# Performance work log

Hardware: AMD Instinct MI355X
Metric: run time of the kernel (lower is better)

## Reference

```python
import jax, jax.numpy as jnp
import numpy as np
import math

E = 1024   # embed_dim
H = 16     # num_heads
D = E // H # head_dim


def _rotary(x):
    # x: [B, H, S, D]. Faithful to the original quirky implementation:
    # pos_enc[:, 0::2] = sin(position * div_term), then cos/sin are taken OF that value.
    S = x.shape[2]
    position = jnp.arange(S, dtype=jnp.float32)[:, None]                     # [S,1]
    div_term = jnp.exp(jnp.arange(0, D, 2, dtype=jnp.float32) * (-math.log(10000.0) / D))  # [D/2]
    angle = jnp.sin(position * div_term)                                     # [S, D/2] == pos_enc[:,0::2]
    cos_t = jnp.cos(angle)                                                   # [S, D/2]
    sin_t = jnp.sin(angle)                                                   # [S, D/2]
    xe = x[..., 0::2]
    xo = x[..., 1::2]
    re = xe * cos_t - xo * sin_t
    ro = xo * cos_t + xe * sin_t
    # interleave even/odd back: [..., D/2, 2] -> [..., D]
    return jnp.stack([re, ro], axis=-1).reshape(x.shape)


def setup_inputs() -> dict:
    key = jax.random.key(0)
    ks = jax.random.split(key, 12)
    B, S = 4, 1024
    scale = 1.0 / math.sqrt(E)
    inp = {
        "query": jax.random.normal(ks[0], (B, S, E), dtype=jnp.float32),
        "key":   jax.random.normal(ks[1], (B, S, E), dtype=jnp.float32),
        "value": jax.random.normal(ks[2], (B, S, E), dtype=jnp.float32),
        # Linear params stored as [in, out]; y = x @ W + b
        "Wq": jax.random.normal(ks[3], (E, E), dtype=jnp.float32) * scale,
        "bq": jnp.zeros((E,), dtype=jnp.float32),
        "Wk": jax.random.normal(ks[4], (E, E), dtype=jnp.float32) * scale,
        "bk": jnp.zeros((E,), dtype=jnp.float32),
        "Wv": jax.random.normal(ks[5], (E, E), dtype=jnp.float32) * scale,
        "bv": jnp.zeros((E,), dtype=jnp.float32),
        "Wo": jax.random.normal(ks[6], (E, E), dtype=jnp.float32) * scale,
        "bo": jnp.zeros((E,), dtype=jnp.float32),
    }
    return inp


def reference(query, key, value, Wq, bq, Wk, bk, Wv, bv, Wo, bo):
    B, S, _ = query.shape
    # projections -> [B, H, S, D]
    q = (query @ Wq + bq).reshape(B, S, H, D).transpose(0, 2, 1, 3)
    k = (key   @ Wk + bk).reshape(B, S, H, D).transpose(0, 2, 1, 3)
    v = (value @ Wv + bv).reshape(B, S, H, D).transpose(0, 2, 1, 3)
    q = _rotary(q)
    k = _rotary(k)
    scores = jnp.einsum('bhsd,bhtd->bhst', q, k) / (D ** 0.5)  # [B,H,S,S]
    probs = jax.nn.softmax(scores, axis=-1)
    # dropout p=0 (eval) -> identity
    ctx = jnp.einsum('bhst,bhtd->bhsd', probs, v)              # [B,H,S,D]
    ctx = ctx.transpose(0, 2, 1, 3).reshape(B, S, E)
    out = ctx @ Wo + bo
    return out, probs
```

## Files before the change

kernel.cpp:

```cpp
#include <hip/hip_runtime.h>
#include <hip/hip_bf16.h>

typedef __attribute__((ext_vector_type(8))) short bf16x8;
typedef __attribute__((ext_vector_type(4))) float f32x4;
typedef unsigned short u16;

__device__ __forceinline__ u16 f2bf(float f) {
  unsigned u = __float_as_uint(f);
  u += 0x7fffu + ((u >> 16) & 1u);
  return (u16)(u >> 16);
}

__device__ __forceinline__ void gload16(const void* g, void* l) {
  __builtin_amdgcn_global_load_lds(
      (const __attribute__((address_space(1))) unsigned int*)g,
      (__attribute__((address_space(3))) unsigned int*)l, 16, 0, 0);
}

__device__ __forceinline__ void blockbar() {
  asm volatile("" ::: "memory");
  __builtin_amdgcn_s_barrier();
  asm volatile("" ::: "memory");
}

__global__ __launch_bounds__(256) void prep_kernel(
    const float* __restrict__ query, const float* __restrict__ key_,
    const float* __restrict__ value, u16* __restrict__ qin,
    u16* __restrict__ kin, u16* __restrict__ vin,
    const float* __restrict__ Wq, const float* __restrict__ Wk,
    const float* __restrict__ Wv, const float* __restrict__ Wo,
    u16* __restrict__ WqT, u16* __restrict__ WkT, u16* __restrict__ WvT,
    u16* __restrict__ WoT, float* __restrict__ cosT, float* __restrict__ sinT) {
  __shared__ float tile[32][33];
  const int z = blockIdx.z;
  const int bx = blockIdx.x;
  const int tid = threadIdx.x;
  if (z < 3) {
    const float* in = z == 0 ? query : z == 1 ? key_ : value;
    u16* out = z == 0 ? qin : z == 1 ? kin : vin;
    size_t i = ((size_t)bx * 256 + tid) * 4;
    float4 v = *(const float4*)(in + i);
    ushort4 o = make_ushort4(f2bf(v.x), f2bf(v.y), f2bf(v.z), f2bf(v.w));
    *(ushort4*)(out + i) = o;
  } else if (z == 3) {
    const int w = bx >> 10;
    const float* W = w == 0 ? Wq : w == 1 ? Wk : w == 2 ? Wv : Wo;
    u16* Wt = w == 0 ? WqT : w == 1 ? WkT : w == 2 ? WvT : WoT;
    int tx = tid & 31, ty = tid >> 5;
    int k0 = ((bx >> 5) & 31) * 32, n0 = (bx & 31) * 32;
#pragma unroll
    for (int i = 0; i < 4; ++i)
      tile[ty + i * 8][tx] = W[(size_t)(k0 + ty + i * 8) * 1024 + n0 + tx];
    __syncthreads();
#pragma unroll
    for (int i = 0; i < 4; ++i)
      Wt[(size_t)(n0 + ty + i * 8) * 1024 + k0 + tx] = f2bf(tile[tx][ty + i * 8]);
  } else {
    int i = bx * 256 + tid;
    if (i >= 1024 * 32) return;
    int s = i >> 5, p = i & 31;
    double freq = exp(-9.210340371976184 * (double)(2 * p) / 64.0);
    double ang = sin((double)s * freq);
    cosT[i] = (float)cos(ang);
    sinT[i] = (float)sin(ang);
  }
}

__global__ __launch_bounds__(256) void proj_gemm_kernel(
    const u16* __restrict__ qin, const u16* __restrict__ kin,
    const u16* __restrict__ vin, const u16* __restrict__ WqT,
    const u16* __restrict__ WkT, const u16* __restrict__ WvT,
    const float* __restrict__ bq, const float* __restrict__ bk,
    const float* __restrict__ bv, u16* __restrict__ qr, u16* __restrict__ kr,
    u16* __restrict__ vt, const float* __restrict__ cosT,
    const float* __restrict__ sinT) {
  __shared__ u16 lA[2][128 * 32];
  __shared__ u16 lB[2][128 * 32];
  const int z = blockIdx.z;
  const u16* A = z == 0 ? qin : z == 1 ? kin : vin;
  const u16* Bt = z == 0 ? WqT : z == 1 ? WkT : WvT;
  const float* bias = z == 0 ? bq : z == 1 ? bk : bv;

  const int tid = threadIdx.x;
  const int lane = tid & 63, wid = tid >> 6;
  const int wm = wid >> 1, wn = wid & 1;
  const int lr = lane & 15, kg = lane >> 4;
  const int m0 = blockIdx.y * 128, n0 = blockIdx.x * 128;

  auto stage = [&](int bu, int k0) {
#pragma unroll
    for (int it = 0; it < 2; ++it) {
      int o = tid * 16 + it * 4096;
      int row = o >> 6;
      int cbs = (((o >> 4) & 3) ^ (row & 3)) << 4;
      gload16((const char*)A + ((size_t)(m0 + row) * 1024 + k0) * 2 + cbs,
              (char*)lA[bu] + o);
      gload16((const char*)Bt + ((size_t)(n0 + row) * 1024 + k0) * 2 + cbs,
              (char*)lB[bu] + o);
    }
  };

  stage(0, 0);
  f32x4 acc[4][4] = {};
  for (int t = 0; t < 32; ++t) {
    if (t < 31) {
      stage((t + 1) & 1, (t + 1) * 32);
      asm volatile("s_waitcnt vmcnt(4)" ::: "memory");
    } else {
      asm volatile("s_waitcnt vmcnt(0)" ::: "memory");
    }
    blockbar();
    const int cb = t & 1;
    bf16x8 av[4], bv_[4];
#pragma unroll
    for (int i = 0; i < 4; ++i) {
      int ra = wm * 64 + i * 16 + lr;
      av[i] = *(const bf16x8*)((const char*)lA[cb] + ra * 64 + ((kg ^ (ra & 3)) << 4));
      int rb = wn * 64 + i * 16 + lr;
      bv_[i] = *(const bf16x8*)((const char*)lB[cb] + rb * 64 + ((kg ^ (rb & 3)) << 4));
    }
#pragma unroll
    for (int i = 0; i < 4; ++i)
#pragma unroll
      for (int j = 0; j < 4; ++j)
        acc[i][j] = __builtin_amdgcn_mfma_f32_16x16x32_bf16(av[i], bv_[j], acc[i][j], 0, 0, 0);
    blockbar();
  }

  if (z == 2) {
    const int bb = m0 >> 10;
#pragma unroll
    for (int i = 0; i < 4; ++i) {
      int srow = (m0 & 1023) + wm * 64 + i * 16 + kg * 4;
#pragma unroll
      for (int j = 0; j < 4; ++j) {
        int col = n0 + wn * 64 + j * 16 + lr;
        float bcol = bias[col];
        int h = col >> 6, d = col & 63;
        ushort4 o;
        o.x = f2bf(acc[i][j][0] + bcol);
        o.y = f2bf(acc[i][j][1] + bcol);
        o.z = f2bf(acc[i][j][2] + bcol);
        o.w = f2bf(acc[i][j][3] + bcol);
        *(ushort4*)(vt + ((size_t)((bb * 16 + h) * 64 + d)) * 1024 + srow) = o;
      }
    }
  } else {
    u16* Cout = z == 0 ? qr : kr;
#pragma unroll
    for (int i = 0; i < 4; ++i) {
#pragma unroll
      for (int j = 0; j < 4; ++j) {
        int col = n0 + wn * 64 + j * 16 + lr;
        float bcol = bias[col];
#pragma unroll
        for (int r = 0; r < 4; ++r) {
          int row = m0 + wm * 64 + i * 16 + kg * 4 + r;
          float v = acc[i][j][r] + bcol;
          float pv = __shfl_xor(v, 1);
          int p = (col & 63) >> 1;
          int s = row & 1023;
          float ct = cosT[s * 32 + p], st = sinT[s * 32 + p];
          float ov = (col & 1) ? (v * ct + pv * st) : (v * ct - pv * st);
          Cout[(size_t)row * 1024 + col] = f2bf(ov);
        }
      }
    }
  }
}

__global__ __launch_bounds__(256) void out_gemm_kernel(
    const u16* __restrict__ A, const u16* __restrict__ Bt,
    const float* __restrict__ bias, float* __restrict__ Cout) {
  __shared__ u16 lA[2][128 * 32];
  __shared__ u16 lB[2][128 * 32];
  const int tid = threadIdx.x;
  const int lane = tid & 63, wid = tid >> 6;
  const int wm = wid >> 1, wn = wid & 1;
  const int lr = lane & 15, kg = lane >> 4;
  const int m0 = blockIdx.y * 128, n0 = blockIdx.x * 128;

  auto stage = [&](int bu, int k0) {
#pragma unroll
    for (int it = 0; it < 2; ++it) {
      int o = tid * 16 + it * 4096;
      int row = o >> 6;
      int cbs = (((o >> 4) & 3) ^ (row & 3)) << 4;
      gload16((const char*)A + ((size_t)(m0 + row) * 1024 + k0) * 2 + cbs,
              (char*)lA[bu] + o);
      gload16((const char*)Bt + ((size_t)(n0 + row) * 1024 + k0) * 2 + cbs,
              (char*)lB[bu] + o);
    }
  };

  stage(0, 0);
  f32x4 acc[4][4] = {};
  for (int t = 0; t < 32; ++t) {
    if (t < 31) {
      stage((t + 1) & 1, (t + 1) * 32);
      asm volatile("s_waitcnt vmcnt(4)" ::: "memory");
    } else {
      asm volatile("s_waitcnt vmcnt(0)" ::: "memory");
    }
    blockbar();
    const int cb = t & 1;
    bf16x8 av[4], bv_[4];
#pragma unroll
    for (int i = 0; i < 4; ++i) {
      int ra = wm * 64 + i * 16 + lr;
      av[i] = *(const bf16x8*)((const char*)lA[cb] + ra * 64 + ((kg ^ (ra & 3)) << 4));
      int rb = wn * 64 + i * 16 + lr;
      bv_[i] = *(const bf16x8*)((const char*)lB[cb] + rb * 64 + ((kg ^ (rb & 3)) << 4));
    }
#pragma unroll
    for (int i = 0; i < 4; ++i)
#pragma unroll
      for (int j = 0; j < 4; ++j)
        acc[i][j] = __builtin_amdgcn_mfma_f32_16x16x32_bf16(av[i], bv_[j], acc[i][j], 0, 0, 0);
    blockbar();
  }
#pragma unroll
  for (int i = 0; i < 4; ++i)
#pragma unroll
    for (int j = 0; j < 4; ++j) {
      int col = n0 + wn * 64 + j * 16 + lr;
      float bcol = bias[col];
#pragma unroll
      for (int r = 0; r < 4; ++r) {
        int row = m0 + wm * 64 + i * 16 + kg * 4 + r;
        Cout[(size_t)row * 1024 + col] = acc[i][j][r] + bcol;
      }
    }
}

__global__ __launch_bounds__(512, 4) void fused_attn_kernel(
    const u16* __restrict__ qr, const u16* __restrict__ kr,
    const u16* __restrict__ vt, float* __restrict__ probs,
    u16* __restrict__ ctx) {
  __shared__ u16 lQ[32 * 64];
  __shared__ u16 lK[2][128 * 64];
  __shared__ u16 lV[2][64 * 128];
  __shared__ u16 lP[32 * 128];
  __shared__ float redM[8][32];
  __shared__ float redS[8][32];

  const int tid = threadIdx.x;
  const int lane = tid & 63, wid = tid >> 6;
  const int lr = lane & 15, kg = lane >> 4;
  const int z = blockIdx.x, b = z >> 4, h = z & 15;
  const int m0 = blockIdx.y * 32;

  const char* Qb = (const char*)qr + ((size_t)(b * 1024 + m0) * 1024 + h * 64) * 2;
  const char* Kb = (const char*)kr + ((size_t)(b * 1024) * 1024 + h * 64) * 2;
  const char* Vb = (const char*)vt + (size_t)z * 64 * 1024 * 2;

  auto stageK = [&](int bu, int c) {
#pragma unroll
    for (int it = 0; it < 2; ++it) {
      int o = tid * 16 + it * 8192;
      int row = o >> 7, ch = (o >> 4) & 7;
      gload16(Kb + (size_t)(c * 128 + row) * 2048 + ((ch ^ (row & 7)) << 4),
              (char*)lK[bu] + o);
    }
  };
  auto stageV = [&](int bu, int c) {
#pragma unroll
    for (int it = 0; it < 2; ++it) {
      int o = tid * 16 + it * 8192;
      int row = o >> 8, ch = (o >> 4) & 15;
      gload16(Vb + (size_t)row * 2048 + c * 256 + ((ch ^ (row & 15)) << 4),
              (char*)lV[bu] + o);
    }
  };

  if (tid < 256) {
    int o = tid * 16;
    int row = o >> 7, ch = (o >> 4) & 7;
    gload16(Qb + (size_t)row * 2048 + ((ch ^ (row & 7)) << 4), (char*)lQ + o);
  }
  stageK(0, 0);

  bf16x8 qf[2][2];
  f32x4 accS[8][2] = {};
#pragma unroll
  for (int c = 0; c < 8; ++c) {
    if (c < 7) {
      stageK((c + 1) & 1, c + 1);
      asm volatile("s_waitcnt vmcnt(2)" ::: "memory");
    } else {
      asm volatile("s_waitcnt vmcnt(0)" ::: "memory");
    }
    blockbar();
    if (c == 0) {
#pragma unroll
      for (int ii = 0; ii < 2; ++ii)
#pragma unroll
        for (int ks = 0; ks < 2; ++ks) {
          int ra = ii * 16 + lr;
          int cc = ks * 4 + kg;
          qf[ii][ks] = *(const bf16x8*)((const char*)lQ + ra * 128 + ((cc ^ (ra & 7)) << 4));
        }
    }
    __builtin_amdgcn_s_setprio(1);
#pragma unroll
    for (int ks = 0; ks < 2; ++ks) {
      int rb = wid * 16 + lr;
      bf16x8 kf =
          *(const bf16x8*)((const char*)lK[c & 1] + rb * 128 + (((ks * 4 + kg) ^ (rb & 7)) << 4));
#pragma unroll
      for (int ii = 0; ii < 2; ++ii)
        accS[c][ii] =
            __builtin_amdgcn_mfma_f32_16x16x32_bf16(qf[ii][ks], kf, accS[c][ii], 0, 0, 0);
    }
    __builtin_amdgcn_s_setprio(0);
    blockbar();
  }

  stageV(0, 0);

  float rmax[2][4];
#pragma unroll
  for (int ii = 0; ii < 2; ++ii)
#pragma unroll
    for (int r = 0; r < 4; ++r) rmax[ii][r] = -1e30f;
#pragma unroll
  for (int c = 0; c < 8; ++c)
#pragma unroll
    for (int ii = 0; ii < 2; ++ii)
#pragma unroll
      for (int r = 0; r < 4; ++r) {
        float v = accS[c][ii][r] * 0.125f;
        accS[c][ii][r] = v;
        rmax[ii][r] = fmaxf(rmax[ii][r], v);
      }
#pragma unroll
  for (int ii = 0; ii < 2; ++ii)
#pragma unroll
    for (int r = 0; r < 4; ++r) {
      float v = rmax[ii][r];
      v = fmaxf(v, __shfl_xor(v, 1));
      v = fmaxf(v, __shfl_xor(v, 2));
      v = fmaxf(v, __shfl_xor(v, 4));
      v = fmaxf(v, __shfl_xor(v, 8));
      rmax[ii][r] = v;
    }
  if (lr == 0) {
#pragma unroll
    for (int ii = 0; ii < 2; ++ii)
#pragma unroll
      for (int r = 0; r < 4; ++r) redM[wid][ii * 16 + kg * 4 + r] = rmax[ii][r];
  }
  asm volatile("s_waitcnt lgkmcnt(0)" ::: "memory");
  blockbar();
  float rowm[2][4], rsum[2][4];
#pragma unroll
  for (int ii = 0; ii < 2; ++ii)
#pragma unroll
    for (int r = 0; r < 4; ++r) {
      int row = ii * 16 + kg * 4 + r;
      float m01 = fmaxf(redM[0][row], redM[1][row]);
      float m23 = fmaxf(redM[2][row], redM[3][row]);
      float m45 = fmaxf(redM[4][row], redM[5][row]);
      float m67 = fmaxf(redM[6][row], redM[7][row]);
      rowm[ii][r] = fmaxf(fmaxf(m01, m23), fmaxf(m45, m67));
      rsum[ii][r] = 0.f;
    }
#pragma unroll
  for (int c = 0; c < 8; ++c)
#pragma unroll
    for (int ii = 0; ii < 2; ++ii)
#pragma unroll
      for (int r = 0; r < 4; ++r) {
        float e = __expf(accS[c][ii][r] - rowm[ii][r]);
        accS[c][ii][r] = e;
        rsum[ii][r] += e;
      }
#pragma unroll
  for (int ii = 0; ii < 2; ++ii)
#pragma unroll
    for (int r = 0; r < 4; ++r) {
      float v = rsum[ii][r];
      v += __shfl_xor(v, 1);
      v += __shfl_xor(v, 2);
      v += __shfl_xor(v, 4);
      v += __shfl_xor(v, 8);
      rsum[ii][r] = v;
    }
  if (lr == 0) {
#pragma unroll
    for (int ii = 0; ii < 2; ++ii)
#pragma unroll
      for (int r = 0; r < 4; ++r) redS[wid][ii * 16 + kg * 4 + r] = rsum[ii][r];
  }
  asm volatile("s_waitcnt lgkmcnt(0)" ::: "memory");
  blockbar();
  float inv[2][4];
#pragma unroll
  for (int ii = 0; ii < 2; ++ii)
#pragma unroll
    for (int r = 0; r < 4; ++r) {
      int row = ii * 16 + kg * 4 + r;
      float s = redS[0][row] + redS[1][row] + redS[2][row] + redS[3][row] +
                redS[4][row] + redS[5][row] + redS[6][row] + redS[7][row];
      inv[ii][r] = 1.0f / s;
    }

  const int ipv = wid >> 2, jpv = wid & 3;
  f32x4 accPV = {};
  float* Pg = probs + (size_t)z * 1024 * 1024 + (size_t)m0 * 1024;

#pragma unroll
  for (int c = 0; c < 8; ++c) {
    if (c < 7) stageV((c + 1) & 1, c + 1);
#pragma unroll
    for (int ii = 0; ii < 2; ++ii)
#pragma unroll
      for (int r = 0; r < 4; ++r) {
        float p = accS[c][ii][r] * inv[ii][r];
        int row = ii * 16 + kg * 4 + r;
        int col = wid * 16 + lr;
        Pg[(size_t)row * 1024 + c * 128 + col] = p;
        *(u16*)((char*)lP + row * 256 + ((((col >> 3) ^ (row & 15))) << 4) + (col & 7) * 2) =
            f2bf(p);
      }
    if (c < 7)
      asm volatile("s_waitcnt vmcnt(18) lgkmcnt(0)" ::: "memory");
    else
      asm volatile("s_waitcnt vmcnt(16) lgkmcnt(0)" ::: "memory");
    blockbar();
    __builtin_amdgcn_s_setprio(1);
#pragma unroll
    for (int ks = 0; ks < 4; ++ks) {
      int cc = ks * 4 + kg;
      int ra = ipv * 16 + lr;
      bf16x8 pa = *(const bf16x8*)((const char*)lP + ra * 256 + ((cc ^ (ra & 15)) << 4));
      int rb = jpv * 16 + lr;
      bf16x8 vbf = *(const bf16x8*)((const char*)lV[c & 1] + rb * 256 + ((cc ^ (rb & 15)) << 4));
      accPV = __builtin_amdgcn_mfma_f32_16x16x32_bf16(pa, vbf, accPV, 0, 0, 0);
    }
    __builtin_amdgcn_s_setprio(0);
    blockbar();
  }

#pragma unroll
  for (int r = 0; r < 4; ++r) {
    int row = m0 + ipv * 16 + kg * 4 + r;
    int d = jpv * 16 + lr;
    ctx[((size_t)(b * 1024 + row)) * 1024 + h * 64 + d] = f2bf(accPV[r]);
  }
}

extern "C" void kernel_launch(void* const* d_in, const int* in_sizes, int n_in,
                              void* d_out, int out_size, void* d_ws, size_t ws_size,
                              hipStream_t stream) {
  const float* query = (const float*)d_in[0];
  const float* key_ = (const float*)d_in[1];
  const float* value = (const float*)d_in[2];
  const float* Wq = (const float*)d_in[3];
  const float* bq = (const float*)d_in[4];
  const float* Wk = (const float*)d_in[5];
  const float* bk = (const float*)d_in[6];
  const float* Wv = (const float*)d_in[7];
  const float* bv = (const float*)d_in[8];
  const float* Wo = (const float*)d_in[9];
  const float* bo = (const float*)d_in[10];

  float* out = (float*)d_out;
  float* probs = out + (size_t)4 * 1024 * 1024;

  char* w = (char*)d_ws;
  const size_t SZ_MK = (size_t)4096 * 1024 * 2;
  const size_t SZ_W = (size_t)1024 * 1024 * 2;
  u16* qin = (u16*)w; w += SZ_MK;
  u16* kin = (u16*)w; w += SZ_MK;
  u16* vin = (u16*)w; w += SZ_MK;
  u16* qr = (u16*)w; w += SZ_MK;
  u16* kr = (u16*)w; w += SZ_MK;
  u16* vt = (u16*)w; w += SZ_MK;
  u16* WqT = (u16*)w; w += SZ_W;
  u16* WkT = (u16*)w; w += SZ_W;
  u16* WvT = (u16*)w; w += SZ_W;
  u16* WoT = (u16*)w; w += SZ_W;
  float* cosT = (float*)w; w += 1024 * 32 * 4;
  float* sinT = (float*)w; w += 1024 * 32 * 4;
  u16* ctx = qin;

  dim3 blk(256);
  hipLaunchKernelGGL(prep_kernel, dim3(4096, 1, 5), blk, 0, stream,
                     query, key_, value, qin, kin, vin, Wq, Wk, Wv, Wo,
                     WqT, WkT, WvT, WoT, cosT, sinT);
  hipLaunchKernelGGL(proj_gemm_kernel, dim3(8, 32, 3), blk, 0, stream,
                     qin, kin, vin, WqT, WkT, WvT, bq, bk, bv, qr, kr, vt,
                     cosT, sinT);
  hipLaunchKernelGGL(fused_attn_kernel, dim3(64, 32), dim3(512), 0, stream,
                     qr, kr, vt, probs, ctx);
  hipLaunchKernelGGL(out_gemm_kernel, dim3(8, 32), blk, 0, stream,
                     ctx, WoT, bo, out);
}
```

Baseline: 194.6 us.

## Load Q, K, V fragments directly from global memory instead of LDS staging

Removes the double-buffered LDS staging of Q, K and V tiles via global_load_lds, along with the associated barriers and waitcnt bookkeeping. MFMA operands are now read straight from global memory into registers. This frees LDS, which may allow higher occupancy, and drops per-chunk synchronisation, but it gives up the prefetch overlap. The global reads are strided 16-byte per-lane accesses that rely on L2/cache hits, and K/V tiles are no longer shared through LDS within the block.

New measurement: 241.5 us. +24.1%, slower.

```diff
diff --git a/kernel.cpp b/kernel.cpp
--- a/kernel.cpp
+++ b/kernel.cpp
@@ -237,9 +237,6 @@
     const u16* __restrict__ qr, const u16* __restrict__ kr,
     const u16* __restrict__ vt, float* __restrict__ probs,
     u16* __restrict__ ctx) {
-  __shared__ u16 lQ[32 * 64];
-  __shared__ u16 lK[2][128 * 64];
-  __shared__ u16 lV[2][64 * 128];
   __shared__ u16 lP[32 * 128];
   __shared__ float redM[8][32];
   __shared__ float redS[8][32];
@@ -254,69 +251,27 @@
   const char* Kb = (const char*)kr + ((size_t)(b * 1024) * 1024 + h * 64) * 2;
   const char* Vb = (const char*)vt + (size_t)z * 64 * 1024 * 2;
 
-  auto stageK = [&](int bu, int c) {
-#pragma unroll
-    for (int it = 0; it < 2; ++it) {
-      int o = tid * 16 + it * 8192;
-      int row = o >> 7, ch = (o >> 4) & 7;
-      gload16(Kb + (size_t)(c * 128 + row) * 2048 + ((ch ^ (row & 7)) << 4),
-              (char*)lK[bu] + o);
-    }
-  };
-  auto stageV = [&](int bu, int c) {
-#pragma unroll
-    for (int it = 0; it < 2; ++it) {
-      int o = tid * 16 + it * 8192;
-      int row = o >> 8, ch = (o >> 4) & 15;
-      gload16(Vb + (size_t)row * 2048 + c * 256 + ((ch ^ (row & 15)) << 4),
-              (char*)lV[bu] + o);
-    }
-  };
-
-  if (tid < 256) {
-    int o = tid * 16;
-    int row = o >> 7, ch = (o >> 4) & 7;
-    gload16(Qb + (size_t)row * 2048 + ((ch ^ (row & 7)) << 4), (char*)lQ + o);
-  }
-  stageK(0, 0);
-
   bf16x8 qf[2][2];
+#pragma unroll
+  for (int ii = 0; ii < 2; ++ii)
+#pragma unroll
+    for (int ks = 0; ks < 2; ++ks)
+      qf[ii][ks] =
+          *(const bf16x8*)(Qb + (size_t)(ii * 16 + lr) * 2048 + (ks * 4 + kg) * 16);
+
   f32x4 accS[8][2] = {};
 #pragma unroll
   for (int c = 0; c < 8; ++c) {
-    if (c < 7) {
-      stageK((c + 1) & 1, c + 1);
-      asm volatile("s_waitcnt vmcnt(2)" ::: "memory");
-    } else {
-      asm volatile("s_waitcnt vmcnt(0)" ::: "memory");
-    }
-    blockbar();
-    if (c == 0) {
-#pragma unroll
-      for (int ii = 0; ii < 2; ++ii)
-#pragma unroll
-        for (int ks = 0; ks < 2; ++ks) {
-          int ra = ii * 16 + lr;
-          int cc = ks * 4 + kg;
-          qf[ii][ks] = *(const bf16x8*)((const char*)lQ + ra * 128 + ((cc ^ (ra & 7)) << 4));
-        }
-    }
-    __builtin_amdgcn_s_setprio(1);
 #pragma unroll
     for (int ks = 0; ks < 2; ++ks) {
-      int rb = wid * 16 + lr;
-      bf16x8 kf =
-          *(const bf16x8*)((const char*)lK[c & 1] + rb * 128 + (((ks * 4 + kg) ^ (rb & 7)) << 4));
+      int rb = c * 128 + wid * 16 + lr;
+      bf16x8 kf = *(const bf16x8*)(Kb + (size_t)rb * 2048 + (ks * 4 + kg) * 16);
 #pragma unroll
       for (int ii = 0; ii < 2; ++ii)
         accS[c][ii] =
             __builtin_amdgcn_mfma_f32_16x16x32_bf16(qf[ii][ks], kf, accS[c][ii], 0, 0, 0);
     }
-    __builtin_amdgcn_s_setprio(0);
-    blockbar();
-  }
-
-  stageV(0, 0);
+  }
 
   float rmax[2][4];
 #pragma unroll
@@ -411,7 +366,6 @@
 
 #pragma unroll
   for (int c = 0; c < 8; ++c) {
-    if (c < 7) stageV((c + 1) & 1, c + 1);
 #pragma unroll
     for (int ii = 0; ii < 2; ++ii)
 #pragma unroll
@@ -423,10 +377,7 @@
         *(u16*)((char*)lP + row * 256 + ((((col >> 3) ^ (row & 15))) << 4) + (col & 7) * 2) =
             f2bf(p);
       }
-    if (c < 7)
-      asm volatile("s_waitcnt vmcnt(18) lgkmcnt(0)" ::: "memory");
-    else
-      asm volatile("s_waitcnt vmcnt(16) lgkmcnt(0)" ::: "memory");
+    asm volatile("s_waitcnt lgkmcnt(0)" ::: "memory");
     blockbar();
     __builtin_amdgcn_s_setprio(1);
 #pragma unroll
@@ -435,7 +386,7 @@
       int ra = ipv * 16 + lr;
       bf16x8 pa = *(const bf16x8*)((const char*)lP + ra * 256 + ((cc ^ (ra & 15)) << 4));
       int rb = jpv * 16 + lr;
-      bf16x8 vbf = *(const bf16x8*)((const char*)lV[c & 1] + rb * 256 + ((cc ^ (rb & 15)) << 4));
+      bf16x8 vbf = *(const bf16x8*)(Vb + (size_t)rb * 2048 + c * 256 + cc * 16);
       accPV = __builtin_amdgcn_mfma_f32_16x16x32_bf16(pa, vbf, accPV, 0, 0, 0);
     }
     __builtin_amdgcn_s_setprio(0);
```
